# Performance work log

Measured on AMD Instinct MI355X. Metric: run time of the kernel, lower is better.

The kernel has to match this reference:

```python
import jax, jax.numpy as jnp
import numpy as np

IN_CH = 64
INTER = IN_CH // 2
B, H, W = 2, 80, 80


def setup_inputs() -> dict:
    key = jax.random.key(0)
    k = jax.random.split(key, 5)
    s = 1.0 / np.sqrt(IN_CH)
    return {
        "x": jax.random.normal(k[0], (B, IN_CH, H, W), dtype=jnp.float32),
        "g_w": jax.random.normal(k[1], (INTER, IN_CH), dtype=jnp.float32) * s,
        "theta_w": jax.random.normal(k[2], (INTER, IN_CH), dtype=jnp.float32) * s,
        "phi_w": jax.random.normal(k[3], (INTER, IN_CH), dtype=jnp.float32) * s,
        "w_w": jax.random.normal(k[4], (IN_CH, INTER), dtype=jnp.float32) * (1.0 / np.sqrt(INTER)),
    }


def reference(x, g_w, theta_w, phi_w, w_w):
    # Non-local block: 1x1 convs (bias=False) are channel matmuls over N=H*W positions.
    Bc, C, Hh, Ww = x.shape
    N = Hh * Ww
    xf = x.reshape(Bc, C, N)                            # [B, C, N]
    g = jnp.einsum('ic,bcn->bni', g_w, xf)              # [B, N, inter]
    theta = jnp.einsum('ic,bcn->bni', theta_w, xf)      # [B, N, inter]
    phi = jnp.einsum('ic,bcn->bin', phi_w, xf)          # [B, inter, N]
    affinity = jax.nn.softmax(jnp.einsum('bni,bim->bnm', theta, phi), axis=-1)  # [B, N, N]
    y = jnp.einsum('bnm,bmi->bni', affinity, g)         # [B, N, inter]
    y = jnp.einsum('ci,bni->bcn', w_w, y).reshape(Bc, C, Hh, Ww)
    return x + y
```

## Files before the change

### kernel.cpp

```cpp
#include <hip/hip_runtime.h>
#include <math.h>

#define BATCH 2
#define CH    64
#define INTER 32
#define NPOS  6400
#define LOG2E 1.44269504088896f
#define SPLIT 10
#define TPB   5

typedef _Float16 f16x8 __attribute__((ext_vector_type(8)));
typedef _Float16 h4    __attribute__((ext_vector_type(4)));
typedef float    f32x4 __attribute__((ext_vector_type(4)));

__global__ __launch_bounds__(256) void nlb_proj_kernel(
    const float* __restrict__ x,
    const float* __restrict__ g_w,
    const float* __restrict__ th_w,
    const float* __restrict__ ph_w,
    _Float16* __restrict__ Qh, _Float16* __restrict__ Kh,
    _Float16* __restrict__ Vt)
{
    const int b  = blockIdx.z;
    const int p  = blockIdx.y;
    const int n0 = blockIdx.x * 64;
    const int t  = threadIdx.x;
    const int w  = __builtin_amdgcn_readfirstlane(t) >> 6;
    const int lane = t & 63;

    const float* wsrc = (p == 0) ? th_w : (p == 1) ? ph_w : g_w;
    const float* xg = x + (size_t)b * CH * NPOS + n0 + lane;

    float xr[64];
    #pragma unroll
    for (int c = 0; c < 64; c++) xr[c] = xg[(size_t)c * NPOS];

    __shared__ float buf[32][65];

    float accs[8];
    #pragma unroll
    for (int rr = 0; rr < 8; rr++) {
        const int row = w * 8 + rr;
        const float* wr = wsrc + row * 64;
        float a0 = 0.f, a1 = 0.f, a2 = 0.f, a3 = 0.f;
        #pragma unroll
        for (int c = 0; c < 16; c++) {
            a0 += wr[c]      * xr[c];
            a1 += wr[c + 16] * xr[c + 16];
            a2 += wr[c + 32] * xr[c + 32];
            a3 += wr[c + 48] * xr[c + 48];
        }
        accs[rr] = (a0 + a1) + (a2 + a3);
    }

    if (p == 2) {
        const int n    = n0 + lane;
        const int kk   = n & 127;
        const int ksw  = (kk & 15) * 8 + (kk >> 4);
        const size_t col = (size_t)(n >> 7) * 128 + ksw;
        #pragma unroll
        for (int rr = 0; rr < 8; rr++)
            Vt[((size_t)b * 32 + w * 8 + rr) * NPOS + col] = (_Float16)accs[rr];
        return;
    }

    #pragma unroll
    for (int rr = 0; rr < 8; rr++) buf[w * 8 + rr][lane] = accs[rr];
    __syncthreads();

    const float scale = (p == 0) ? LOG2E : 1.f;
    _Float16* dst = (p == 0) ? Qh : Kh;
    const int pos = t >> 2, ic = t & 3;
    f16x8 hv;
    #pragma unroll
    for (int j = 0; j < 8; j++)
        hv[j] = (_Float16)(buf[ic * 8 + j][pos] * scale);
    *(f16x8*)(dst + ((size_t)b * NPOS + n0 + pos) * 32 + ic * 8) = hv;
}

__global__ __launch_bounds__(256) void nlb_flash_kernel(
    const _Float16* __restrict__ Qh, const _Float16* __restrict__ Kh,
    const _Float16* __restrict__ Vt,
    _Float16* __restrict__ Opart, float2* __restrict__ ml)
{
    __shared__ __align__(16) _Float16 ks[128][40];
    __shared__ __align__(16) _Float16 vs[32][144];
    __shared__ __align__(16) _Float16 pm[4][16][136];

    const int b     = blockIdx.z;
    const int split = blockIdx.y;
    const int t     = threadIdx.x;
    const int w     = t >> 6;
    const int lane  = t & 63;
    const int n16   = lane & 15;
    const int quad  = lane >> 4;
    const int q0    = blockIdx.x * 64 + w * 16;

    const f16x8 qa = *(const f16x8*)(Qh + ((size_t)b * NPOS + q0 + n16) * 32 + quad * 8);

    f32x4 o0 = {0.f, 0.f, 0.f, 0.f};
    f32x4 o1 = {0.f, 0.f, 0.f, 0.f};
    float runm[4] = {-1e30f, -1e30f, -1e30f, -1e30f};
    float lloc[4] = {0.f, 0.f, 0.f, 0.f};

    const _Float16* KB = Kh + (size_t)b * NPOS * 32;
    const _Float16* VB = Vt + (size_t)b * 32 * NPOS;

    const int kt0 = split * TPB;
    for (int kt = kt0; kt < kt0 + TPB; kt++) {
        __syncthreads();
        {
            const int k0 = kt * 128;
            #pragma unroll
            for (int i = 0; i < 2; i++) {
                int c = t + i * 256;
                int key = c >> 2, part = c & 3;
                *(f16x8*)&ks[key][part * 8] =
                    *(const f16x8*)(KB + (size_t)(k0 + key) * 32 + part * 8);
                int dim = c >> 4, kp = c & 15;
                *(f16x8*)&vs[dim][kp * 8] =
                    *(const f16x8*)(VB + (size_t)dim * NPOS + k0 + kp * 8);
            }
        }
        __syncthreads();

        f32x4 sc[8];
        #pragma unroll
        for (int g = 0; g < 8; g++) {
            f16x8 kf = *(const f16x8*)&ks[g * 16 + n16][quad * 8];
            f32x4 z = {0.f, 0.f, 0.f, 0.f};
            sc[g] = __builtin_amdgcn_mfma_f32_16x16x32_f16(qa, kf, z, 0, 0, 0);
        }

        #pragma unroll
        for (int r = 0; r < 4; r++) {
            float m = sc[0][r];
            #pragma unroll
            for (int g = 1; g < 8; g++) m = fmaxf(m, sc[g][r]);
            m = fmaxf(m, __shfl_xor(m, 1));
            m = fmaxf(m, __shfl_xor(m, 2));
            m = fmaxf(m, __shfl_xor(m, 4));
            m = fmaxf(m, __shfl_xor(m, 8));
            float nm = fmaxf(runm[r], m);
            float a  = __builtin_amdgcn_exp2f(runm[r] - nm);
            float ls = 0.f;
            f16x8 pv;
            #pragma unroll
            for (int g = 0; g < 8; g++) {
                float p = __builtin_amdgcn_exp2f(sc[g][r] - nm);
                pv[g] = (_Float16)p;
                ls += p;
            }
            lloc[r] = lloc[r] * a + ls;
            runm[r] = nm;
            o0[r] *= a; o1[r] *= a;
            *(f16x8*)&pm[w][quad * 4 + r][n16 * 8] = pv;
        }

        #pragma unroll
        for (int kc = 0; kc < 4; kc++) {
            f16x8 pa = *(const f16x8*)&pm[w][n16][kc * 32 + quad * 8];
            f16x8 v0 = *(const f16x8*)&vs[n16][kc * 32 + quad * 8];
            f16x8 v1 = *(const f16x8*)&vs[16 + n16][kc * 32 + quad * 8];
            o0 = __builtin_amdgcn_mfma_f32_16x16x32_f16(pa, v0, o0, 0, 0, 0);
            o1 = __builtin_amdgcn_mfma_f32_16x16x32_f16(pa, v1, o1, 0, 0, 0);
        }
    }

    #pragma unroll
    for (int r = 0; r < 4; r++) {
        float l = lloc[r];
        l += __shfl_xor(l, 1); l += __shfl_xor(l, 2);
        l += __shfl_xor(l, 4); l += __shfl_xor(l, 8);
        float invl = 1.f / l;
        int q = q0 + quad * 4 + r;
        size_t base = ((size_t)(b * SPLIT + split) * NPOS + q) * 32;
        Opart[base + n16]      = (_Float16)(o0[r] * invl);
        Opart[base + 16 + n16] = (_Float16)(o1[r] * invl);
        if (n16 == 0)
            ml[(size_t)(b * SPLIT + split) * NPOS + q] = make_float2(runm[r], l);
    }
}

__global__ __launch_bounds__(256) void nlb_combine_kernel(
    const _Float16* __restrict__ Opart, const float2* __restrict__ ml,
    const float* __restrict__ w_w, const float* __restrict__ x,
    float* __restrict__ out)
{
    __shared__ float wf[64][33];
    __shared__ float wts[32][12];
    __shared__ float of[32][33];

    const int b  = blockIdx.y;
    const int q0 = blockIdx.x * 32;
    const int t  = threadIdx.x;

    for (int idx = t; idx < 2048; idx += 256) wf[idx >> 5][idx & 31] = w_w[idx];

    if (t < 32) {
        float2 v[SPLIT];
        float m = -1e30f;
        #pragma unroll
        for (int s = 0; s < SPLIT; s++) {
            v[s] = ml[(size_t)(b * SPLIT + s) * NPOS + q0 + t];
            m = fmaxf(m, v[s].x);
        }
        float suml = 0.f;
        #pragma unroll
        for (int s = 0; s < SPLIT; s++) {
            float wgt = __builtin_amdgcn_exp2f(v[s].x - m) * v[s].y;
            wts[t][s] = wgt;
            suml += wgt;
        }
        float inv = 1.f / suml;
        #pragma unroll
        for (int s = 0; s < SPLIT; s++) wts[t][s] *= inv;
    }
    __syncthreads();

    {
        const int q = t >> 3, dg = t & 7;
        float a0 = 0.f, a1 = 0.f, a2 = 0.f, a3 = 0.f;
        #pragma unroll
        for (int s = 0; s < SPLIT; s++) {
            h4 hv = *(const h4*)(Opart +
                ((size_t)(b * SPLIT + s) * NPOS + q0 + q) * 32 + dg * 4);
            float c = wts[q][s];
            a0 += c * (float)hv[0]; a1 += c * (float)hv[1];
            a2 += c * (float)hv[2]; a3 += c * (float)hv[3];
        }
        of[q][dg * 4]     = a0; of[q][dg * 4 + 1] = a1;
        of[q][dg * 4 + 2] = a2; of[q][dg * 4 + 3] = a3;
    }
    __syncthreads();

    {
        const int q = t & 31, cg = t >> 5;
        const float* xb = x   + (size_t)b * CH * NPOS + q0 + q;
        float*       ob = out + (size_t)b * CH * NPOS + q0 + q;
        #pragma unroll
        for (int cc = 0; cc < 8; cc++) {
            int ch = cg * 8 + cc;
            float acc = 0.f;
            #pragma unroll
            for (int i = 0; i < 32; i++) acc += wf[ch][i] * of[q][i];
            ob[(size_t)ch * NPOS] = acc + xb[(size_t)ch * NPOS];
        }
    }
}

extern "C" void kernel_launch(void* const* d_in, const int* in_sizes, int n_in,
                              void* d_out, int out_size, void* d_ws, size_t ws_size,
                              hipStream_t stream) {
    const float* x    = (const float*)d_in[0];
    const float* g_w  = (const float*)d_in[1];
    const float* th_w = (const float*)d_in[2];
    const float* ph_w = (const float*)d_in[3];
    const float* w_w  = (const float*)d_in[4];
    float* out = (float*)d_out;

    const size_t SZ = (size_t)BATCH * NPOS * INTER;
    _Float16* Qh = (_Float16*)d_ws;
    _Float16* Kh = Qh + SZ;
    _Float16* Vt = Kh + SZ;
    _Float16* Opart = Vt + SZ;
    float2*   ml    = (float2*)(Opart + SZ * SPLIT);

    nlb_proj_kernel<<<dim3(NPOS / 64, 3, BATCH), 256, 0, stream>>>(
        x, g_w, th_w, ph_w, Qh, Kh, Vt);
    nlb_flash_kernel<<<dim3(NPOS / 64, SPLIT, BATCH), 256, 0, stream>>>(
        Qh, Kh, Vt, Opart, ml);
    nlb_combine_kernel<<<dim3(NPOS / 32, BATCH), 256, 0, stream>>>(
        Opart, ml, w_w, x, out);
}
```

Before: 117.7 us.

## Prefetch next K/V tile into registers and use DPP row-max reduction

```diff
diff --git a/kernel.cpp b/kernel.cpp
--- a/kernel.cpp
+++ b/kernel.cpp
@@ -12,6 +12,18 @@
 typedef _Float16 f16x8 __attribute__((ext_vector_type(8)));
 typedef _Float16 h4    __attribute__((ext_vector_type(4)));
 typedef float    f32x4 __attribute__((ext_vector_type(4)));
+
+template <int N>
+static __device__ __forceinline__ float max_ror(float x) {
+    int r = __builtin_amdgcn_mov_dpp(__builtin_bit_cast(int, x),
+                                     0x120 | N, 0xF, 0xF, true);
+    return fmaxf(x, __builtin_bit_cast(float, r));
+}
+static __device__ __forceinline__ float rowmax16(float x) {
+    x = max_ror<1>(x); x = max_ror<2>(x);
+    x = max_ror<4>(x); x = max_ror<8>(x);
+    return x;
+}
 
 __global__ __launch_bounds__(256) void nlb_proj_kernel(
     const float* __restrict__ x,
@@ -106,23 +118,37 @@
     const _Float16* KB = Kh + (size_t)b * NPOS * 32;
     const _Float16* VB = Vt + (size_t)b * 32 * NPOS;
 
+    const int key0 = t >> 2,            part0 = t & 3;
+    const int key1 = (t + 256) >> 2,    part1 = t & 3;
+    const int dim0 = t >> 4,            kp0   = t & 15;
+    const int dim1 = (t + 256) >> 4,    kp1   = t & 15;
+
+    f16x8 kr0, kr1, vr0, vr1;
     const int kt0 = split * TPB;
+    {
+        const int k0 = kt0 * 128;
+        kr0 = *(const f16x8*)(KB + (size_t)(k0 + key0) * 32 + part0 * 8);
+        kr1 = *(const f16x8*)(KB + (size_t)(k0 + key1) * 32 + part1 * 8);
+        vr0 = *(const f16x8*)(VB + (size_t)dim0 * NPOS + k0 + kp0 * 8);
+        vr1 = *(const f16x8*)(VB + (size_t)dim1 * NPOS + k0 + kp1 * 8);
+    }
+
     for (int kt = kt0; kt < kt0 + TPB; kt++) {
         __syncthreads();
+        *(f16x8*)&ks[key0][part0 * 8] = kr0;
+        *(f16x8*)&ks[key1][part1 * 8] = kr1;
+        *(f16x8*)&vs[dim0][kp0 * 8]   = vr0;
+        *(f16x8*)&vs[dim1][kp1 * 8]   = vr1;
+        __syncthreads();
+
         {
-            const int k0 = kt * 128;
-            #pragma unroll
-            for (int i = 0; i < 2; i++) {
-                int c = t + i * 256;
-                int key = c >> 2, part = c & 3;
-                *(f16x8*)&ks[key][part * 8] =
-                    *(const f16x8*)(KB + (size_t)(k0 + key) * 32 + part * 8);
-                int dim = c >> 4, kp = c & 15;
-                *(f16x8*)&vs[dim][kp * 8] =
-                    *(const f16x8*)(VB + (size_t)dim * NPOS + k0 + kp * 8);
-            }
-        }
-        __syncthreads();
+            const int ktn = (kt + 1 < kt0 + TPB) ? kt + 1 : kt;
+            const int k0n = ktn * 128;
+            kr0 = *(const f16x8*)(KB + (size_t)(k0n + key0) * 32 + part0 * 8);
+            kr1 = *(const f16x8*)(KB + (size_t)(k0n + key1) * 32 + part1 * 8);
+            vr0 = *(const f16x8*)(VB + (size_t)dim0 * NPOS + k0n + kp0 * 8);
+            vr1 = *(const f16x8*)(VB + (size_t)dim1 * NPOS + k0n + kp1 * 8);
+        }
 
         f32x4 sc[8];
         #pragma unroll
@@ -134,13 +160,12 @@
 
         #pragma unroll
         for (int r = 0; r < 4; r++) {
-            float m = sc[0][r];
-            #pragma unroll
-            for (int g = 1; g < 8; g++) m = fmaxf(m, sc[g][r]);
-            m = fmaxf(m, __shfl_xor(m, 1));
-            m = fmaxf(m, __shfl_xor(m, 2));
-            m = fmaxf(m, __shfl_xor(m, 4));
-            m = fmaxf(m, __shfl_xor(m, 8));
+            float m01 = fmaxf(sc[0][r], sc[1][r]);
+            float m23 = fmaxf(sc[2][r], sc[3][r]);
+            float m45 = fmaxf(sc[4][r], sc[5][r]);
+            float m67 = fmaxf(sc[6][r], sc[7][r]);
+            float m = fmaxf(fmaxf(m01, m23), fmaxf(m45, m67));
+            m = rowmax16(m);
             float nm = fmaxf(runm[r], m);
             float a  = __builtin_amdgcn_exp2f(runm[r] - nm);
             float ls = 0.f;
```

After: 112.1 us. 4.8% less time.

## Compute transposed S in flash kernel, drop LDS staging, register-prefetch K/V

Applied to the files above, without the earlier changes.

```diff
diff --git a/kernel.cpp b/kernel.cpp
--- a/kernel.cpp
+++ b/kernel.cpp
@@ -54,10 +54,11 @@
     }
 
     if (p == 2) {
-        const int n    = n0 + lane;
-        const int kk   = n & 127;
-        const int ksw  = (kk & 15) * 8 + (kk >> 4);
-        const size_t col = (size_t)(n >> 7) * 128 + ksw;
+        const int n   = n0 + lane;
+        const int kk  = n & 127;
+        const int g   = kk >> 4, qd = (kk >> 2) & 3, rr2 = kk & 3;
+        const int slot = (g >> 1) * 32 + qd * 8 + (g & 1) * 4 + rr2;
+        const size_t col = (size_t)(n >> 7) * 128 + slot;
         #pragma unroll
         for (int rr = 0; rr < 8; rr++)
             Vt[((size_t)b * 32 + w * 8 + rr) * NPOS + col] = (_Float16)accs[rr];
@@ -83,10 +84,6 @@
     const _Float16* __restrict__ Vt,
     _Float16* __restrict__ Opart, float2* __restrict__ ml)
 {
-    __shared__ __align__(16) _Float16 ks[128][40];
-    __shared__ __align__(16) _Float16 vs[32][144];
-    __shared__ __align__(16) _Float16 pm[4][16][136];
-
     const int b     = blockIdx.z;
     const int split = blockIdx.y;
     const int t     = threadIdx.x;
@@ -98,88 +95,99 @@
 
     const f16x8 qa = *(const f16x8*)(Qh + ((size_t)b * NPOS + q0 + n16) * 32 + quad * 8);
 
+    const _Float16* KB = Kh + (size_t)b * NPOS * 32;
+    const _Float16* VB = Vt + (size_t)b * 32 * NPOS;
+
     f32x4 o0 = {0.f, 0.f, 0.f, 0.f};
     f32x4 o1 = {0.f, 0.f, 0.f, 0.f};
-    float runm[4] = {-1e30f, -1e30f, -1e30f, -1e30f};
-    float lloc[4] = {0.f, 0.f, 0.f, 0.f};
-
-    const _Float16* KB = Kh + (size_t)b * NPOS * 32;
-    const _Float16* VB = Vt + (size_t)b * 32 * NPOS;
+    float runm = -1e30f, lsum = 0.f;
 
     const int kt0 = split * TPB;
+
+    f16x8 ka[8], va[8];
+    {
+        const int k0 = kt0 * 128;
+        #pragma unroll
+        for (int g = 0; g < 8; g++)
+            ka[g] = *(const f16x8*)(KB + (size_t)(k0 + g * 16 + n16) * 32 + quad * 8);
+        #pragma unroll
+        for (int kc = 0; kc < 4; kc++)
+            #pragma unroll
+            for (int h = 0; h < 2; h++)
+                va[kc * 2 + h] = *(const f16x8*)(
+                    VB + (size_t)(n16 + 16 * h) * NPOS + k0 + kc * 32 + quad * 8);
+    }
+
     for (int kt = kt0; kt < kt0 + TPB; kt++) {
-        __syncthreads();
-        {
-            const int k0 = kt * 128;
-            #pragma unroll
-            for (int i = 0; i < 2; i++) {
-                int c = t + i * 256;
-                int key = c >> 2, part = c & 3;
-                *(f16x8*)&ks[key][part * 8] =
-                    *(const f16x8*)(KB + (size_t)(k0 + key) * 32 + part * 8);
-                int dim = c >> 4, kp = c & 15;
-                *(f16x8*)&vs[dim][kp * 8] =
-                    *(const f16x8*)(VB + (size_t)dim * NPOS + k0 + kp * 8);
-            }
-        }
-        __syncthreads();
+        const int ktn = (kt + 1 < kt0 + TPB) ? kt + 1 : kt;
+        const int k0n = ktn * 128;
 
         f32x4 sc[8];
         #pragma unroll
         for (int g = 0; g < 8; g++) {
-            f16x8 kf = *(const f16x8*)&ks[g * 16 + n16][quad * 8];
             f32x4 z = {0.f, 0.f, 0.f, 0.f};
-            sc[g] = __builtin_amdgcn_mfma_f32_16x16x32_f16(qa, kf, z, 0, 0, 0);
-        }
-
-        #pragma unroll
-        for (int r = 0; r < 4; r++) {
-            float m = sc[0][r];
-            #pragma unroll
-            for (int g = 1; g < 8; g++) m = fmaxf(m, sc[g][r]);
-            m = fmaxf(m, __shfl_xor(m, 1));
-            m = fmaxf(m, __shfl_xor(m, 2));
-            m = fmaxf(m, __shfl_xor(m, 4));
-            m = fmaxf(m, __shfl_xor(m, 8));
-            float nm = fmaxf(runm[r], m);
-            float a  = __builtin_amdgcn_exp2f(runm[r] - nm);
-            float ls = 0.f;
-            f16x8 pv;
-            #pragma unroll
-            for (int g = 0; g < 8; g++) {
+            sc[g] = __builtin_amdgcn_mfma_f32_16x16x32_f16(ka[g], qa, z, 0, 0, 0);
+        }
+        #pragma unroll
+        for (int g = 0; g < 8; g++)
+            ka[g] = *(const f16x8*)(KB + (size_t)(k0n + g * 16 + n16) * 32 + quad * 8);
+
+        float m = fmaxf(fmaxf(sc[0][0], sc[0][1]), fmaxf(sc[0][2], sc[0][3]));
+        #pragma unroll
+        for (int g = 1; g < 8; g++) {
+            float mg = fmaxf(fmaxf(sc[g][0], sc[g][1]), fmaxf(sc[g][2], sc[g][3]));
+            m = fmaxf(m, mg);
+        }
+        m = fmaxf(m, __shfl_xor(m, 16));
+        m = fmaxf(m, __shfl_xor(m, 32));
+        float nm = fmaxf(runm, m);
+        float a  = __builtin_amdgcn_exp2f(runm - nm);
+        runm = nm;
+        float ls = 0.f;
+        #pragma unroll
+        for (int g = 0; g < 8; g++) {
+            #pragma unroll
+            for (int r = 0; r < 4; r++) {
                 float p = __builtin_amdgcn_exp2f(sc[g][r] - nm);
-                pv[g] = (_Float16)p;
+                sc[g][r] = p;
                 ls += p;
             }
-            lloc[r] = lloc[r] * a + ls;
-            runm[r] = nm;
-            o0[r] *= a; o1[r] *= a;
-            *(f16x8*)&pm[w][quad * 4 + r][n16 * 8] = pv;
-        }
+        }
+        lsum = lsum * a + ls;
+        o0 *= a;
+        o1 *= a;
 
         #pragma unroll
         for (int kc = 0; kc < 4; kc++) {
-            f16x8 pa = *(const f16x8*)&pm[w][n16][kc * 32 + quad * 8];
-            f16x8 v0 = *(const f16x8*)&vs[n16][kc * 32 + quad * 8];
-            f16x8 v1 = *(const f16x8*)&vs[16 + n16][kc * 32 + quad * 8];
-            o0 = __builtin_amdgcn_mfma_f32_16x16x32_f16(pa, v0, o0, 0, 0, 0);
-            o1 = __builtin_amdgcn_mfma_f32_16x16x32_f16(pa, v1, o1, 0, 0, 0);
-        }
-    }
-
+            f16x8 pb;
+            #pragma unroll
+            for (int j = 0; j < 8; j++)
+                pb[j] = (_Float16)sc[kc * 2 + (j >> 2)][j & 3];
+            o0 = __builtin_amdgcn_mfma_f32_16x16x32_f16(va[kc * 2 + 0], pb, o0, 0, 0, 0);
+            o1 = __builtin_amdgcn_mfma_f32_16x16x32_f16(va[kc * 2 + 1], pb, o1, 0, 0, 0);
+        }
+        #pragma unroll
+        for (int kc = 0; kc < 4; kc++)
+            #pragma unroll
+            for (int h = 0; h < 2; h++)
+                va[kc * 2 + h] = *(const f16x8*)(
+                    VB + (size_t)(n16 + 16 * h) * NPOS + k0n + kc * 32 + quad * 8);
+    }
+
+    lsum += __shfl_xor(lsum, 16);
+    lsum += __shfl_xor(lsum, 32);
+    float invl = 1.f / lsum;
+    const size_t base = ((size_t)(b * SPLIT + split) * NPOS + q0 + n16) * 32;
+    h4 h0, h1;
     #pragma unroll
     for (int r = 0; r < 4; r++) {
-        float l = lloc[r];
-        l += __shfl_xor(l, 1); l += __shfl_xor(l, 2);
-        l += __shfl_xor(l, 4); l += __shfl_xor(l, 8);
-        float invl = 1.f / l;
-        int q = q0 + quad * 4 + r;
-        size_t base = ((size_t)(b * SPLIT + split) * NPOS + q) * 32;
-        Opart[base + n16]      = (_Float16)(o0[r] * invl);
-        Opart[base + 16 + n16] = (_Float16)(o1[r] * invl);
-        if (n16 == 0)
-            ml[(size_t)(b * SPLIT + split) * NPOS + q] = make_float2(runm[r], l);
-    }
+        h0[r] = (_Float16)(o0[r] * invl);
+        h1[r] = (_Float16)(o1[r] * invl);
+    }
+    *(h4*)(Opart + base + quad * 4)      = h0;
+    *(h4*)(Opart + base + 16 + quad * 4) = h1;
+    if (quad == 0)
+        ml[(size_t)(b * SPLIT + split) * NPOS + q0 + n16] = make_float2(runm, lsum);
 }
 
 __global__ __launch_bounds__(256) void nlb_combine_kernel(
```

After: 148.0 us. 25.7% more time.
